# Performance work log

Measured on AMD Instinct MI355X. Metric: run time of the kernel, lower is better.

Reference implementation:

```python
import jax, jax.numpy as jnp
import numpy as np

NUM_HEADS = 16
ENCODE_DIM = 1024
KEY_DIM = 64
VALUE_DIM = 64
B, T = 2, 2048
NEG_INF = -1e30  # large negative instead of -inf for grad safety; same softmax result


def setup_inputs() -> dict:
    key = jax.random.key(0)
    ks = jax.random.split(key, 8)
    s_in = 1.0 / np.sqrt(ENCODE_DIM)
    s_out = 1.0 / np.sqrt(NUM_HEADS * VALUE_DIM)
    return {
        "K": jax.random.normal(ks[0], (B, T, ENCODE_DIM), jnp.float32),
        "Q": jax.random.normal(ks[1], (B, T, ENCODE_DIM), jnp.float32),
        "V": jax.random.normal(ks[2], (B, T, ENCODE_DIM), jnp.float32),
        # per-head projection weights stacked along head axis: [H, C, d]
        "Wk": jax.random.normal(ks[3], (NUM_HEADS, ENCODE_DIM, KEY_DIM), jnp.float32) * s_in,
        "Wq": jax.random.normal(ks[4], (NUM_HEADS, ENCODE_DIM, KEY_DIM), jnp.float32) * s_in,
        "Wv": jax.random.normal(ks[5], (NUM_HEADS, ENCODE_DIM, VALUE_DIM), jnp.float32) * s_in,
        # output projection: concat over heads -> encode_dim, with bias
        "Wo": jax.random.normal(ks[6], (NUM_HEADS * VALUE_DIM, ENCODE_DIM), jnp.float32) * s_out,
        "bo": jax.random.normal(ks[7], (ENCODE_DIM,), jnp.float32) * 0.01,
    }


def reference(K, Q, V, Wk, Wq, Wv, Wo, bo):
    # Batched per-head projections (original loops over heads with separate Linears)
    k = jnp.einsum('btc,hcd->bhtd', K, Wk)  # [B,H,T,dk]
    q = jnp.einsum('btc,hcd->bhtd', Q, Wq)  # [B,H,T,dk]
    v = jnp.einsum('btc,hcd->bhtd', V, Wv)  # [B,H,T,dv]
    scores = jnp.einsum('bhtd,bhsd->bhts', q, k)  # [B,H,T,T]
    t = scores.shape[-1]
    causal = jnp.tril(jnp.ones((t, t), bool))
    scores = jnp.where(causal, scores, NEG_INF)
    # original: mask first, then scale by 1/sqrt(key_dim), then softmax
    attn = jax.nn.softmax(scores * (1.0 / (KEY_DIM ** 0.5)), axis=-1)
    # dropout is identity in eval mode
    out = jnp.einsum('bhts,bhsd->bhtd', attn, v)  # [B,H,T,dv]
    b, h, tt, dv = out.shape
    concat = out.transpose(0, 2, 1, 3).reshape(b, tt, h * dv)  # head concat order matches loop
    return concat @ Wo + bo
```

## Files before the change

### kernel.cpp

```cpp
#include <hip/hip_runtime.h>
#include <hip/hip_bf16.h>

typedef __bf16 bf16_t;
typedef __bf16 bf16x4 __attribute__((ext_vector_type(4)));
typedef __bf16 bf16x8 __attribute__((ext_vector_type(8)));
typedef float f32x4 __attribute__((ext_vector_type(4)));
typedef int i32x2 __attribute__((ext_vector_type(2)));
typedef unsigned int u32;

static __device__ __forceinline__ u32 pk2(float a, float b) {
    union { u32 u; bf16_t h[2]; } w;
    w.h[0] = (bf16_t)a; w.h[1] = (bf16_t)b;
    return w.u;
}

static __device__ __forceinline__ float fold32_add(float x) {
    i32x2 r = __builtin_amdgcn_permlane32_swap(__float_as_int(x), __float_as_int(x),
                                               false, false);
    return __int_as_float(r[0]) + __int_as_float(r[1]);
}

#define GLOAD_LDS16(gsrc, ldst)                                                  \
    __builtin_amdgcn_global_load_lds(                                            \
        (const __attribute__((address_space(1))) void*)(gsrc),                   \
        (__attribute__((address_space(3))) void*)(ldst), 16, 0, 0)

__global__ void conv_w_all(const float* __restrict__ Wq, const float* __restrict__ Wk,
                           const float* __restrict__ Wv, const float* __restrict__ Wo,
                           bf16_t* __restrict__ Oq, bf16_t* __restrict__ Ok,
                           bf16_t* __restrict__ Ov, bf16_t* __restrict__ Oo) {
    __shared__ bf16_t t[64][72];
    const int z = blockIdx.z;
    const int tid = threadIdx.x;
    if (z < 3) {
        const float* in = (z == 0) ? Wq : (z == 1) ? Wk : Wv;
        bf16_t* out = (z == 0) ? Oq : (z == 1) ? Ok : Ov;
        const int tc = blockIdx.x, h = blockIdx.y;
#pragma unroll
        for (int p = 0; p < 4; ++p) {
            int r = p * 16 + (tid >> 4);
            int c4 = (tid & 15) * 4;
            float4 x = *(const float4*)(in + (size_t)h * 65536 + (size_t)(tc * 64 + r) * 64 + c4);
            t[r][c4 + 0] = (bf16_t)x.x; t[r][c4 + 1] = (bf16_t)x.y;
            t[r][c4 + 2] = (bf16_t)x.z; t[r][c4 + 3] = (bf16_t)x.w;
        }
        __syncthreads();
#pragma unroll
        for (int p = 0; p < 2; ++p) {
            int d = p * 32 + (tid >> 3);
            int c8 = (tid & 7) * 8;
            bf16x8 v;
#pragma unroll
            for (int j = 0; j < 8; ++j) v[j] = t[c8 + j][d];
            *(bf16x8*)(out + (size_t)(h * 64 + d) * 1024 + tc * 64 + c8) = v;
        }
    } else {
        const int r0 = blockIdx.x * 64;
        const int c0 = blockIdx.y * 64;
#pragma unroll
        for (int p = 0; p < 4; ++p) {
            int r = p * 16 + (tid >> 4);
            int c4 = (tid & 15) * 4;
            float4 x = *(const float4*)(Wo + (size_t)(r0 + r) * 1024 + c0 + c4);
            t[r][c4 + 0] = (bf16_t)x.x; t[r][c4 + 1] = (bf16_t)x.y;
            t[r][c4 + 2] = (bf16_t)x.z; t[r][c4 + 3] = (bf16_t)x.w;
        }
        __syncthreads();
#pragma unroll
        for (int p = 0; p < 2; ++p) {
            int d = p * 32 + (tid >> 3);
            int c8 = (tid & 7) * 8;
            bf16x8 v;
#pragma unroll
            for (int j = 0; j < 8; ++j) v[j] = t[c8 + j][d];
            *(bf16x8*)(Oo + (size_t)(c0 + d) * 1024 + r0 + c8) = v;
        }
    }
}

template<int BM, bool A_F32, bool OUT_F32, bool BIAS>
__device__ __forceinline__
void gemm_core(const void* Ap, const bf16_t* Bt, void* Cp, const float* bias,
               int m0, int n0, bf16_t* vtout) {
    constexpr int N = 1024, K = 1024, BK = 32;
    constexpr int APAD = A_F32 ? 8 : 0;
    constexpr int MI = BM / 32;
    __shared__ bf16_t As[2][BM][BK + APAD];
    __shared__ bf16_t Bs[2][128][BK];

    const int tid = threadIdx.x;
    const int wv = tid >> 6, l = tid & 63;
    const int ln16 = l & 15, g8 = (l >> 4) * 8;
    const int wr = (wv >> 1) * (BM / 2), wc = (wv & 1) * 64;
    const int srow = l >> 2, scol = (l & 3) * 8;

    const float*  Af = (const float*)Ap;
    const bf16_t* Ab = (const bf16_t*)Ap;

    f32x4 zero = {0.f, 0.f, 0.f, 0.f};
    f32x4 acc[MI][4];
#pragma unroll
    for (int i = 0; i < MI; ++i)
#pragma unroll
        for (int j = 0; j < 4; ++j) acc[i][j] = zero;

    auto stage = [&](int buf, int k0) {
#pragma unroll
        for (int i = 0; i < BM / 64; ++i) {
            int row = wv * (BM / 4) + i * 16;
            if constexpr (A_F32) {
                const float* s = Af + (size_t)(m0 + row + srow) * K + k0 + scol;
                float4 x0 = *(const float4*)s;
                float4 x1 = *(const float4*)(s + 4);
                bf16x8 v;
                v[0] = (bf16_t)x0.x; v[1] = (bf16_t)x0.y; v[2] = (bf16_t)x0.z; v[3] = (bf16_t)x0.w;
                v[4] = (bf16_t)x1.x; v[5] = (bf16_t)x1.y; v[6] = (bf16_t)x1.z; v[7] = (bf16_t)x1.w;
                *(bf16x8*)&As[buf][row + srow][scol] = v;
            } else {
                GLOAD_LDS16(Ab + (size_t)(m0 + row + srow) * K + k0 + scol,
                            &As[buf][row][0]);
            }
        }
#pragma unroll
        for (int i = 0; i < 2; ++i) {
            int row = wv * 32 + i * 16;
            GLOAD_LDS16(Bt + (size_t)(n0 + row + srow) * K + k0 + scol,
                        &Bs[buf][row][0]);
        }
    };

    stage(0, 0);
    __syncthreads();
    for (int kt = 0; kt < K / BK; ++kt) {
        int cur = kt & 1;
        if (kt + 1 < K / BK) stage(cur ^ 1, (kt + 1) * BK);
        bf16x8 a[MI], b[4];
#pragma unroll
        for (int i = 0; i < MI; ++i)
            a[i] = *(const bf16x8*)&As[cur][wr + i * 16 + ln16][g8];
#pragma unroll
        for (int i = 0; i < 4; ++i)
            b[i] = *(const bf16x8*)&Bs[cur][wc + i * 16 + ln16][g8];
#pragma unroll
        for (int mi = 0; mi < MI; ++mi)
#pragma unroll
            for (int ni = 0; ni < 4; ++ni)
                acc[mi][ni] = __builtin_amdgcn_mfma_f32_16x16x32_bf16(
                    a[mi], b[ni], acc[mi][ni], 0, 0, 0);
        __syncthreads();
    }

    float*  Cf = (float*)Cp;
    bf16_t* Cb = (bf16_t*)Cp;
    if constexpr (!OUT_F32) {
        if (vtout) {
#pragma unroll
            for (int mi = 0; mi < MI; ++mi)
#pragma unroll
                for (int ni = 0; ni < 4; ++ni) {
                    int rowb = m0 + wr + mi * 16 + (l >> 4) * 4;
                    int col  = n0 + wc + ni * 16 + ln16;
                    int bb = rowb >> 11, tr = rowb & 2047;
                    bf16x4 v4;
#pragma unroll
                    for (int r = 0; r < 4; ++r) v4[r] = (bf16_t)acc[mi][ni][r];
                    *(bf16x4*)(vtout + ((size_t)bb * 1024 + col) * 2048 + tr) = v4;
                }
            return;
        }
    }
#pragma unroll
    for (int mi = 0; mi < MI; ++mi)
#pragma unroll
        for (int ni = 0; ni < 4; ++ni)
#pragma unroll
            for (int r = 0; r < 4; ++r) {
                int row = m0 + wr + mi * 16 + (l >> 4) * 4 + r;
                int col = n0 + wc + ni * 16 + ln16;
                float v = acc[mi][ni][r];
                if constexpr (BIAS) v += bias[col];
                if constexpr (OUT_F32) Cf[(size_t)row * N + col] = v;
                else                   Cb[(size_t)row * N + col] = (bf16_t)v;
            }
}

__global__ __launch_bounds__(256, 3)
void gemm_proj(const float* A0, const float* A1, const float* A2,
               const bf16_t* B0, const bf16_t* B1, const bf16_t* B2,
               bf16_t* C0, bf16_t* C1, bf16_t* vt) {
    int z = blockIdx.z;
    const float* A = (z == 0) ? A0 : (z == 1) ? A1 : A2;
    const bf16_t* B = (z == 0) ? B0 : (z == 1) ? B1 : B2;
    bf16_t* C = (z == 0) ? C0 : (z == 1) ? C1 : nullptr;
    bf16_t* vto = (z == 2) ? vt : nullptr;
    gemm_core<128, true, false, false>(A, B, C, nullptr,
                                       blockIdx.x * 128, blockIdx.y * 128, vto);
}

__global__ __launch_bounds__(256, 4)
void gemm_out(const bf16_t* A, const bf16_t* Bt, void* C, const float* bias) {
    gemm_core<64, false, true, true>(A, Bt, C, bias,
                                     blockIdx.x * 64, blockIdx.y * 128, nullptr);
}

__global__ __launch_bounds__(256, 2)
void attn_causal(const bf16_t* __restrict__ qp, const bf16_t* __restrict__ kp,
                 const bf16_t* __restrict__ vtp, bf16_t* __restrict__ op) {
    constexpr int T = 2048, HC = 1024;
    constexpr float SC2 = 0.18033688011112042f;
    __shared__ u32 Pex[4][32][32];

    const int tid = threadIdx.x;
    const int wid = tid >> 6, ln = tid & 63;
    const int q16 = ln & 15, g = ln >> 4, g8 = g * 8;
    const u32 swz = (u32)(q16 & 7) << 2;

    const int c = blockIdx.x;
    const int bh = c & 31;
    const int j = (c >> 5) & 7;
    const int half = (c >> 8) & 1;
    const int gidx = j * 4 + wid;
    const int strip = half ? (63 - gidx) : gidx;
    const int qbase = strip * 32;
    const int ntiles = strip / 2 + 1;

    const int b = bh >> 4, h = bh & 15;
    const bf16_t* Q  = qp  + (size_t)b * T * HC + (size_t)h * 64;
    const bf16_t* Kg = kp  + (size_t)b * T * HC + (size_t)h * 64;
    const bf16_t* Vt = vtp + (size_t)b * HC * T + (size_t)h * 64 * T;

    int qrow[2];
    bf16x8 qf[2][2];
#pragma unroll
    for (int st = 0; st < 2; ++st) {
        qrow[st] = qbase + st * 16 + q16;
        qf[st][0] = *(const bf16x8*)(Q + (size_t)qrow[st] * HC + g8);
        qf[st][1] = *(const bf16x8*)(Q + (size_t)qrow[st] * HC + 32 + g8);
    }

    float l[2] = {0.f, 0.f};
    f32x4 zero = {0.f, 0.f, 0.f, 0.f};
    f32x4 oacc[2][4];
#pragma unroll
    for (int st = 0; st < 2; ++st)
#pragma unroll
        for (int i = 0; i < 4; ++i) oacc[st][i] = zero;

    bf16x8 ka[4][2];
    bf16x8 va[2][4];
#pragma unroll
    for (int sb = 0; sb < 4; ++sb) {
        const bf16_t* kr = Kg + (size_t)(sb * 16 + q16) * HC;
        ka[sb][0] = *(const bf16x8*)(kr + g8);
        ka[sb][1] = *(const bf16x8*)(kr + 32 + g8);
    }
#pragma unroll
    for (int kc = 0; kc < 2; ++kc)
#pragma unroll
        for (int nf = 0; nf < 4; ++nf)
            va[kc][nf] = *(const bf16x8*)(Vt + (size_t)(nf * 16 + q16) * T
                                          + kc * 32 + g8);

    for (int t = 0; t < ntiles; ++t) {
        const int kv0 = t * 64;
        const bool last = (t == ntiles - 1);
        const int kvn = kv0 + 64;

        float zs[2][4][4];
        __builtin_amdgcn_s_setprio(1);
#pragma unroll
        for (int sb = 0; sb < 4; ++sb) {
            int sbase = kv0 + sb * 16 + 4 * g;
#pragma unroll
            for (int st = 0; st < 2; ++st) {
                f32x4 z = zero;
                z = __builtin_amdgcn_mfma_f32_16x16x32_bf16(ka[sb][0], qf[st][0], z, 0, 0, 0);
                z = __builtin_amdgcn_mfma_f32_16x16x32_bf16(ka[sb][1], qf[st][1], z, 0, 0, 0);
                if (last) {
#pragma unroll
                    for (int r = 0; r < 4; ++r)
                        zs[st][sb][r] = (sbase + r <= qrow[st]) ? z[r] * SC2 : -1.0e30f;
                } else {
#pragma unroll
                    for (int r = 0; r < 4; ++r) zs[st][sb][r] = z[r] * SC2;
                }
            }
        }
        __builtin_amdgcn_s_setprio(0);

#pragma unroll
        for (int sb = 0; sb < 4; ++sb) {
            const bf16_t* kr = Kg + (size_t)(kvn + sb * 16 + q16) * HC;
            ka[sb][0] = *(const bf16x8*)(kr + g8);
            ka[sb][1] = *(const bf16x8*)(kr + 32 + g8);
        }

#pragma unroll
        for (int st = 0; st < 2; ++st) {
            f32x4 ps4 = zero;
#pragma unroll
            for (int sb = 0; sb < 4; ++sb) {
                float e0 = exp2f(zs[st][sb][0]);
                float e1 = exp2f(zs[st][sb][1]);
                float e2 = exp2f(zs[st][sb][2]);
                float e3 = exp2f(zs[st][sb][3]);
                ps4[0] += e0; ps4[1] += e1; ps4[2] += e2; ps4[3] += e3;
                uint2 w;
                w.x = pk2(e0, e1);
                w.y = pk2(e2, e3);
                u32 colA = ((u32)(sb * 8 + 2 * g)) ^ swz;
                *(uint2*)&Pex[wid][st * 16 + q16][colA] = w;
            }
            float psum = ps4[0] + ps4[1] + ps4[2] + ps4[3];
            psum += __shfl_xor(psum, 16, 64);
            l[st] += fold32_add(psum);
        }

        __builtin_amdgcn_s_setprio(1);
#pragma unroll
        for (int kc = 0; kc < 2; ++kc) {
            bf16x8 pa[2];
#pragma unroll
            for (int st = 0; st < 2; ++st) {
                u32 colR = ((u32)(kc * 16 + 4 * g)) ^ swz;
                pa[st] = *(const bf16x8*)&Pex[wid][st * 16 + q16][colR];
            }
#pragma unroll
            for (int nf = 0; nf < 4; ++nf)
#pragma unroll
                for (int st = 0; st < 2; ++st)
                    oacc[st][nf] = __builtin_amdgcn_mfma_f32_16x16x32_bf16(
                        pa[st], va[kc][nf], oacc[st][nf], 0, 0, 0);
        }
        __builtin_amdgcn_s_setprio(0);

#pragma unroll
        for (int kc = 0; kc < 2; ++kc)
#pragma unroll
            for (int nf = 0; nf < 4; ++nf)
                va[kc][nf] = *(const bf16x8*)(Vt + (size_t)(nf * 16 + q16) * T
                                              + kvn + kc * 32 + g8);
    }

    bf16_t* O = op + (size_t)b * T * HC + (size_t)h * 64;
#pragma unroll
    for (int st = 0; st < 2; ++st) {
        int base = qbase + st * 16;
#pragma unroll
        for (int r = 0; r < 4; ++r) {
            float lr = __shfl(l[st], 4 * g + r, 64);
            float inv = 1.0f / lr;
#pragma unroll
            for (int nf = 0; nf < 4; ++nf)
                O[(size_t)(base + 4 * g + r) * HC + nf * 16 + q16] =
                    (bf16_t)(oacc[st][nf][r] * inv);
        }
    }
}


extern "C" void kernel_launch(void* const* d_in, const int* in_sizes, int n_in,
                              void* d_out, int out_size, void* d_ws, size_t ws_size,
                              hipStream_t stream) {
    const float* K_in = (const float*)d_in[0];
    const float* Q_in = (const float*)d_in[1];
    const float* V_in = (const float*)d_in[2];
    const float* Wk   = (const float*)d_in[3];
    const float* Wq   = (const float*)d_in[4];
    const float* Wv   = (const float*)d_in[5];
    const float* Wo   = (const float*)d_in[6];
    const float* bo   = (const float*)d_in[7];

    char* ws = (char*)d_ws;
    const size_t MB = 1024 * 1024;
    bf16_t* Wqt = (bf16_t*)(ws + 0 * MB);
    bf16_t* Wkt = (bf16_t*)(ws + 2 * MB);
    bf16_t* Wvt = (bf16_t*)(ws + 4 * MB);
    bf16_t* Wot = (bf16_t*)(ws + 6 * MB);
    bf16_t* vt  = (bf16_t*)(ws + 8 * MB);
    bf16_t* kp  = (bf16_t*)(ws + 16 * MB);
    bf16_t* ao  = (bf16_t*)(ws + 24 * MB);
    bf16_t* qp  = (bf16_t*)(ws + 32 * MB);

    conv_w_all<<<dim3(16, 16, 4), 256, 0, stream>>>(Wq, Wk, Wv, Wo,
                                                    Wqt, Wkt, Wvt, Wot);

    gemm_proj<<<dim3(32, 8, 3), 256, 0, stream>>>(Q_in, K_in, V_in,
                                                  Wqt, Wkt, Wvt,
                                                  qp, kp, vt);

    attn_causal<<<512, 256, 0, stream>>>(qp, kp, vt, ao);

    gemm_out<<<dim3(64, 8), 256, 0, stream>>>(ao, Wot, d_out, bo);
}
```

Baseline: 137.4 us.

## Share K/V tiles across waves through double-buffered LDS in causal attention

Each wave previously loaded its own K and V^T fragments straight from global memory. Now the whole block cooperatively stages each 64-row K and V tile into double-buffered LDS, prefetching two tiles ahead in registers, and every wave reads its fragments from LDS. This cuts global/L2 traffic for K/V by the number of waves per block. In exchange it adds a block-wide barrier per tile and makes all waves run the block's maximum tile count. Waves with shorter strips therefore compute extra fully masked tiles.

```diff
diff --git a/kernel.cpp b/kernel.cpp
--- a/kernel.cpp
+++ b/kernel.cpp
@@ -208,6 +208,8 @@
                  const bf16_t* __restrict__ vtp, bf16_t* __restrict__ op) {
     constexpr int T = 2048, HC = 1024;
     constexpr float SC2 = 0.18033688011112042f;
+    __shared__ bf16_t Ks[2][64][80];
+    __shared__ bf16_t Vs[2][64][80];
     __shared__ u32 Pex[4][32][32];
 
     const int tid = threadIdx.x;
@@ -223,6 +225,7 @@
     const int strip = half ? (63 - gidx) : gidx;
     const int qbase = strip * 32;
     const int ntiles = strip / 2 + 1;
+    const int bnt = half ? (32 - 2 * j) : (2 * j + 2);
 
     const int b = bh >> 4, h = bh & 15;
     const bf16_t* Q  = qp  + (size_t)b * T * HC + (size_t)h * 64;
@@ -246,37 +249,50 @@
 #pragma unroll
         for (int i = 0; i < 4; ++i) oacc[st][i] = zero;
 
-    bf16x8 ka[4][2];
-    bf16x8 va[2][4];
-#pragma unroll
-    for (int sb = 0; sb < 4; ++sb) {
-        const bf16_t* kr = Kg + (size_t)(sb * 16 + q16) * HC;
-        ka[sb][0] = *(const bf16x8*)(kr + g8);
-        ka[sb][1] = *(const bf16x8*)(kr + 32 + g8);
-    }
-#pragma unroll
-    for (int kc = 0; kc < 2; ++kc)
-#pragma unroll
-        for (int nf = 0; nf < 4; ++nf)
-            va[kc][nf] = *(const bf16x8*)(Vt + (size_t)(nf * 16 + q16) * T
-                                          + kc * 32 + g8);
-
-    for (int t = 0; t < ntiles; ++t) {
+    const int srow = tid >> 2;
+    const int sc0  = (tid & 3) * 16;
+    int4 kreg[2], vreg[2];
+
+    auto stage_load = [&](int t) {
+        const size_t kv = (size_t)t * 64;
+        kreg[0] = *(const int4*)(Kg + (kv + srow) * HC + sc0);
+        kreg[1] = *(const int4*)(Kg + (kv + srow) * HC + sc0 + 8);
+        vreg[0] = *(const int4*)(Vt + (size_t)srow * T + kv + sc0);
+        vreg[1] = *(const int4*)(Vt + (size_t)srow * T + kv + sc0 + 8);
+    };
+    auto stage_write = [&](int buf) {
+        *(int4*)&Ks[buf][srow][sc0]     = kreg[0];
+        *(int4*)&Ks[buf][srow][sc0 + 8] = kreg[1];
+        *(int4*)&Vs[buf][srow][sc0]     = vreg[0];
+        *(int4*)&Vs[buf][srow][sc0 + 8] = vreg[1];
+    };
+
+    stage_load(0);
+    stage_write(0);
+    if (bnt > 1) stage_load(1);
+    __syncthreads();
+
+    for (int t = 0; t < bnt; ++t) {
+        const int cur = t & 1, nxt = cur ^ 1;
         const int kv0 = t * 64;
-        const bool last = (t == ntiles - 1);
-        const int kvn = kv0 + 64;
+        const bool maskt = (t >= ntiles - 1);
+
+        if (t + 1 < bnt) stage_write(nxt);
+        if (t + 2 < bnt) stage_load(t + 2);
 
         float zs[2][4][4];
         __builtin_amdgcn_s_setprio(1);
 #pragma unroll
         for (int sb = 0; sb < 4; ++sb) {
+            bf16x8 kf0 = *(const bf16x8*)&Ks[cur][sb * 16 + q16][g8];
+            bf16x8 kf1 = *(const bf16x8*)&Ks[cur][sb * 16 + q16][32 + g8];
             int sbase = kv0 + sb * 16 + 4 * g;
 #pragma unroll
             for (int st = 0; st < 2; ++st) {
                 f32x4 z = zero;
-                z = __builtin_amdgcn_mfma_f32_16x16x32_bf16(ka[sb][0], qf[st][0], z, 0, 0, 0);
-                z = __builtin_amdgcn_mfma_f32_16x16x32_bf16(ka[sb][1], qf[st][1], z, 0, 0, 0);
-                if (last) {
+                z = __builtin_amdgcn_mfma_f32_16x16x32_bf16(kf0, qf[st][0], z, 0, 0, 0);
+                z = __builtin_amdgcn_mfma_f32_16x16x32_bf16(kf1, qf[st][1], z, 0, 0, 0);
+                if (maskt) {
 #pragma unroll
                     for (int r = 0; r < 4; ++r)
                         zs[st][sb][r] = (sbase + r <= qrow[st]) ? z[r] * SC2 : -1.0e30f;
@@ -287,13 +303,6 @@
             }
         }
         __builtin_amdgcn_s_setprio(0);
-
-#pragma unroll
-        for (int sb = 0; sb < 4; ++sb) {
-            const bf16_t* kr = Kg + (size_t)(kvn + sb * 16 + q16) * HC;
-            ka[sb][0] = *(const bf16x8*)(kr + g8);
-            ka[sb][1] = *(const bf16x8*)(kr + 32 + g8);
-        }
 
 #pragma unroll
         for (int st = 0; st < 2; ++st) {
@@ -326,20 +335,17 @@
                 pa[st] = *(const bf16x8*)&Pex[wid][st * 16 + q16][colR];
             }
 #pragma unroll
-            for (int nf = 0; nf < 4; ++nf)
+            for (int nf = 0; nf < 4; ++nf) {
+                bf16x8 vf = *(const bf16x8*)&Vs[cur][nf * 16 + q16][kc * 32 + g8];
 #pragma unroll
                 for (int st = 0; st < 2; ++st)
                     oacc[st][nf] = __builtin_amdgcn_mfma_f32_16x16x32_bf16(
-                        pa[st], va[kc][nf], oacc[st][nf], 0, 0, 0);
+                        pa[st], vf, oacc[st][nf], 0, 0, 0);
+            }
         }
         __builtin_amdgcn_s_setprio(0);
 
-#pragma unroll
-        for (int kc = 0; kc < 2; ++kc)
-#pragma unroll
-            for (int nf = 0; nf < 4; ++nf)
-                va[kc][nf] = *(const bf16x8*)(Vt + (size_t)(nf * 16 + q16) * T
-                                              + kvn + kc * 32 + g8);
+        __syncthreads();
     }
 
     bf16_t* O = op + (size_t)b * T * HC + (size_t)h * 64;
```

New measurement: 149.5 us. 8.8% more time.
